# Optimization experiments

Measured on AMD Instinct MI355X. Metric: run time of the kernel, lower is better.

Reference implementation:

```python
import jax, jax.numpy as jnp
import numpy as np

N_E = 1024
E_DIM = 256
BETA = 0.25
EMA_LAMBDA = 0.99

def setup_inputs() -> dict:
    key = jax.random.key(0)
    k1, k2 = jax.random.split(key)
    z = jax.random.normal(k1, (32, 2048, E_DIM), dtype=jnp.float32)
    # torch init: uniform(-1/n_e, 1/n_e)
    embedding = jax.random.uniform(k2, (N_E, E_DIM), dtype=jnp.float32,
                                   minval=-1.0 / N_E, maxval=1.0 / N_E)
    N_t = jnp.zeros((N_E,), dtype=jnp.float32)
    m_t = jnp.zeros((N_E, E_DIM), dtype=jnp.float32)
    return {"z": z, "embedding": embedding, "N_t": N_t, "m_t": m_t}

def reference(z, embedding, N_t, m_t):
    zf = z.reshape(-1, E_DIM)  # [N, e_dim]
    # squared L2 distances: ||z||^2 + ||e||^2 - 2 z e^T  -> [N, n_e]
    d = (jnp.sum(zf * zf, axis=1, keepdims=True)
         + jnp.sum(embedding * embedding, axis=1)
         - 2.0 * jnp.matmul(zf, embedding.T))
    idx = jnp.argmin(d, axis=1)  # [N] int

    # EMA statistics (torch does a python loop over unique indices; this is the
    # vectorized equivalent: only codes that were selected get updated).
    counts = jax.ops.segment_sum(jnp.ones_like(idx, dtype=jnp.float32), idx, num_segments=N_E)
    sums = jax.ops.segment_sum(zf, idx, num_segments=N_E)  # [n_e, e_dim]
    selected = counts > 0
    N_t_new = jnp.where(selected, N_t * EMA_LAMBDA + counts * (1.0 - EMA_LAMBDA), N_t)
    m_t_new = jnp.where(selected[:, None], m_t * EMA_LAMBDA + sums * (1.0 - EMA_LAMBDA), m_t)

    z_q = embedding[idx].reshape(z.shape)
    loss = BETA * jnp.mean((jax.lax.stop_gradient(z_q) - z) ** 2)
    z_q_st = z + jax.lax.stop_gradient(z_q - z)  # straight-through

    # perplexity from code usage histogram (== mean of one-hot encodings)
    e_mean = counts / idx.shape[0]
    perplexity = jnp.exp(-jnp.sum(e_mean * jnp.log(e_mean + 1e-10)))
    return (loss, z_q_st, idx, perplexity, N_t_new, m_t_new)
```

## Files before the change

### kernel.cpp

```cpp
#include <hip/hip_runtime.h>
#include <math.h>

#define N_ROWS  65536
#define EDIM    256
#define NE      1024
#define BETA    0.25f
#define LAMBDA  0.99f

#define MARGIN  8e-3f
#define QCAP    2048


#define O_ZQ   1
#define O_IDX  16777217
#define O_PERP 16842753
#define O_NT   16842754
#define O_MT   16843778

typedef __attribute__((ext_vector_type(8))) short short8;
typedef __attribute__((ext_vector_type(4))) float f32x4;

__device__ __forceinline__ unsigned short f2bf(float f) {
    unsigned u = __float_as_uint(f);
    return (unsigned short)((u + 0x7fffu + ((u >> 16) & 1u)) >> 16);
}

__global__ __launch_bounds__(64) void prep_b_kernel(const float* __restrict__ emb,
                                                    unsigned* __restrict__ bfrag_u32,
                                                    float* __restrict__ loss_acc,
                                                    int* __restrict__ cnt) {
    int j = blockIdx.x;
    int l = threadIdx.x;
    float4 v = ((const float4*)(emb + (size_t)j * EDIM))[l];
    unsigned lo = (unsigned)f2bf(v.x) | ((unsigned)f2bf(v.y) << 16);
    unsigned hi = (unsigned)f2bf(v.z) | ((unsigned)f2bf(v.w) << 16);
    int base = ((((j >> 4) * 8 + (l >> 3)) * 64) + ((l >> 1) & 3) * 16 + (j & 15)) * 4
             + 2 * (l & 1);
    bfrag_u32[base]     = lo;
    bfrag_u32[base + 1] = hi;
    if (l == 0) cnt[j] = 0;
    if (j == 0 && l == 0) *loss_acc = 0.0f;
}

__global__ __launch_bounds__(256) void sq_kernel(const float* __restrict__ src,
                                                 float* __restrict__ dst) {
    const int tid = threadIdx.x;
    const int grp = tid >> 4;
    const int q   = tid & 15;
    const int row = blockIdx.x * 16 + grp;
    const int h = q >> 3, j = q & 7;
    const float* __restrict__ p = src + (size_t)row * EDIM + h * 128 + j;
    float acc = __fmul_rn(p[0], p[0]);
    #pragma unroll
    for (int t = 1; t < 16; ++t) {
        float v = p[8 * t];
        acc = __fadd_rn(acc, __fmul_rn(v, v));
    }
    acc = __fadd_rn(acc, __shfl_xor(acc, 1));
    acc = __fadd_rn(acc, __shfl_xor(acc, 2));
    acc = __fadd_rn(acc, __shfl_xor(acc, 4));
    acc = __fadd_rn(acc, __shfl_xor(acc, 8));
    if (q == 0) dst[row] = acc;
}

__global__ __launch_bounds__(256, 3) void argmin_kernel(const float* __restrict__ z,
                                                        const float* __restrict__ emb,
                                                        const float4* __restrict__ bsrc,
                                                        const float* __restrict__ e_sq,
                                                        int* __restrict__ idx_out,
                                                        float* __restrict__ out_zq,
                                                        float* __restrict__ out_idx,
                                                        float* __restrict__ loss_acc,
                                                        int* __restrict__ cnt) {
    __shared__ __align__(16) float4 Bs[2048];
    __shared__ uint2 queue[QCAP];
    __shared__ unsigned long long best_s[128];
    __shared__ int   idx_s[128];
    __shared__ float zsq_s[128];
    __shared__ float rmF_s[128];
    __shared__ float lred[4];
    __shared__ int qcnt;

    const int tid  = threadIdx.x;
    const int wid  = tid >> 6, lane = tid & 63;
    const int l15  = lane & 15, lg = lane >> 4;
    const int row0 = blockIdx.x * 128;
    const int rbase = row0 + wid * 32;

    if (tid < 128) best_s[tid] = ~0ull;
    if (tid == 0) qcnt = 0;

    float4 st[8];
    #pragma unroll
    for (int i = 0; i < 8; ++i) st[i] = bsrc[tid + 256 * i];

    short8 a[2][8];
    #pragma unroll
    for (int rt = 0; rt < 2; ++rt) {
        float zs = 0.f;
        #pragma unroll
        for (int ks = 0; ks < 8; ++ks) {
            const float* zp = z + (size_t)(rbase + rt * 16 + l15) * EDIM + ks * 32 + lg * 8;
            float4 f0 = *(const float4*)zp;
            float4 f1 = *(const float4*)(zp + 4);
            zs += f0.x * f0.x + f0.y * f0.y + f0.z * f0.z + f0.w * f0.w
                + f1.x * f1.x + f1.y * f1.y + f1.z * f1.z + f1.w * f1.w;
            union { short8 s; unsigned short u[8]; } pk;
            pk.u[0] = f2bf(f0.x); pk.u[1] = f2bf(f0.y); pk.u[2] = f2bf(f0.z); pk.u[3] = f2bf(f0.w);
            pk.u[4] = f2bf(f1.x); pk.u[5] = f2bf(f1.y); pk.u[6] = f2bf(f1.z); pk.u[7] = f2bf(f1.w);
            a[rt][ks] = pk.s;
        }
        zs += __shfl_xor(zs, 16);
        zs += __shfl_xor(zs, 32);
        if (lg == 0) zsq_s[wid * 32 + rt * 16 + l15] = zs;
    }

    float rm[2][4];
    #pragma unroll
    for (int rt = 0; rt < 2; ++rt)
        #pragma unroll
        for (int r = 0; r < 4; ++r) rm[rt][r] = 1e30f;

    __syncthreads();

    for (int ch = 0; ch < 16; ++ch) {
        const int cb = ch * 64;
        #pragma unroll
        for (int i = 0; i < 8; ++i) Bs[tid + 256 * i] = st[i];
        __syncthreads();
        if (ch < 15) {
            #pragma unroll
            for (int i = 0; i < 8; ++i) st[i] = bsrc[(ch + 1) * 2048 + tid + 256 * i];
        }

        float eqs[4];
        #pragma unroll
        for (int ct = 0; ct < 4; ++ct) eqs[ct] = e_sq[cb + ct * 16 + l15];

        f32x4 acc[2][4];
        #pragma unroll
        for (int rt = 0; rt < 2; ++rt)
            #pragma unroll
            for (int ct = 0; ct < 4; ++ct) acc[rt][ct] = (f32x4){0.f, 0.f, 0.f, 0.f};

        const short8* Bv = (const short8*)Bs;
        #pragma unroll
        for (int ks = 0; ks < 8; ++ks) {
            #pragma unroll
            for (int ct = 0; ct < 4; ++ct) {
                short8 b = Bv[(ct * 8 + ks) * 64 + lane];
                acc[0][ct] = __builtin_amdgcn_mfma_f32_16x16x32_bf16(a[0][ks], b, acc[0][ct], 0, 0, 0);
                acc[1][ct] = __builtin_amdgcn_mfma_f32_16x16x32_bf16(a[1][ks], b, acc[1][ct], 0, 0, 0);
            }
        }

        #pragma unroll
        for (int rt = 0; rt < 2; ++rt) {
            #pragma unroll
            for (int r = 0; r < 4; ++r) {
                float m = __fsub_rn(eqs[0], __fmul_rn(2.0f, acc[rt][0][r]));
                #pragma unroll
                for (int ct = 1; ct < 4; ++ct) {
                    float t = __fsub_rn(eqs[ct], __fmul_rn(2.0f, acc[rt][ct][r]));
                    m = fminf(m, t);
                }
                m = fminf(m, __shfl_xor(m, 1));
                m = fminf(m, __shfl_xor(m, 2));
                m = fminf(m, __shfl_xor(m, 4));
                m = fminf(m, __shfl_xor(m, 8));
                rm[rt][r] = fminf(rm[rt][r], m);
            }
        }

        #pragma unroll
        for (int rt = 0; rt < 2; ++rt) {
            #pragma unroll
            for (int ct = 0; ct < 4; ++ct) {
                #pragma unroll
                for (int r = 0; r < 4; ++r) {
                    float t = __fsub_rn(eqs[ct], __fmul_rn(2.0f, acc[rt][ct][r]));
                    if (t <= rm[rt][r] + MARGIN) {
                        int rl  = wid * 32 + rt * 16 + lg * 4 + r;
                        int col = cb + ct * 16 + l15;
                        int s = atomicAdd(&qcnt, 1);
                        if (s < QCAP) queue[s] = make_uint2((rl << 10) | col,
                                                            __float_as_uint(t));
                    }
                }
            }
        }
        __syncthreads();
    }

    #pragma unroll
    for (int rt = 0; rt < 2; ++rt)
        #pragma unroll
        for (int r = 0; r < 4; ++r)
            if (l15 == 0) rmF_s[wid * 32 + rt * 16 + lg * 4 + r] = rm[rt][r];
    __syncthreads();

    {
        int nq = qcnt; if (nq > QCAP) nq = QCAP;
        const int g = tid >> 3, q = tid & 7;
        for (int e = g; e < nq; e += 32) {
            uint2 ent = queue[e];
            int rl = ent.x >> 10, col = ent.x & 1023;
            if (__uint_as_float(ent.y) > rmF_s[rl] + MARGIN) continue;
            const float4* zr = (const float4*)(z + (size_t)(row0 + rl) * EDIM);
            const float4* er = (const float4*)(emb + (size_t)col * EDIM);
            float ae = 0.f;
            #pragma unroll
            for (int i = 0; i < 8; ++i) {
                float4 x = zr[q + 8 * i], y = er[q + 8 * i];
                ae = __fmaf_rn(x.x, y.x, ae);
                ae = __fmaf_rn(x.y, y.y, ae);
                ae = __fmaf_rn(x.z, y.z, ae);
                ae = __fmaf_rn(x.w, y.w, ae);
            }
            ae = __fadd_rn(ae, __shfl_xor(ae, 1));
            ae = __fadd_rn(ae, __shfl_xor(ae, 2));
            ae = __fadd_rn(ae, __shfl_xor(ae, 4));
            if (q == 0) {
                float d = __fsub_rn(__fadd_rn(zsq_s[rl], e_sq[col]), __fmul_rn(2.0f, ae));
                unsigned u = __float_as_uint(d);
                u = (u & 0x80000000u) ? ~u : (u | 0x80000000u);
                unsigned long long key = ((unsigned long long)u << 32) | (unsigned)col;
                atomicMin(&best_s[rl], key);
            }
        }
    }

    __syncthreads();
    if (tid < 128) {
        unsigned long long k = best_s[tid];
        int id = (int)(k & 0xffffffffull);
        idx_out[row0 + tid] = id;
        out_idx[row0 + tid] = (float)id;
        idx_s[tid] = id;
        atomicAdd(&cnt[id], 1);
    }
    __syncthreads();

    const float4* e4 = (const float4*)emb;
    for (int i = 0; i < 32; ++i) {
        int flat = tid + i * 256;
        int r = flat >> 6, c4 = flat & 63;
        int id = idx_s[r];
        float4 e = e4[(size_t)id * 64 + c4];
        float* o = out_zq + (size_t)(row0 + r) * EDIM + c4 * 4;
        o[0] = e.x; o[1] = e.y; o[2] = e.z; o[3] = e.w;
    }

    float lp = 0.f;
    if (tid < 128) {
        unsigned m = (unsigned)(best_s[tid] >> 32);
        unsigned bits = (m & 0x80000000u) ? (m & 0x7fffffffu) : ~m;
        lp = __uint_as_float(bits);
    }
    #pragma unroll
    for (int m = 32; m; m >>= 1) lp += __shfl_down(lp, m);
    if (lane == 0) lred[wid] = lp;
    __syncthreads();
    if (tid == 0) {
        float s = lred[0] + lred[1] + lred[2] + lred[3];
        atomicAdd(loss_acc, s);
    }
}

__global__ __launch_bounds__(1024) void scan_kernel(const int* __restrict__ cnt,
                                                    const float* __restrict__ N_t,
                                                    float* __restrict__ outN,
                                                    float* __restrict__ counts_f,
                                                    int* __restrict__ offs,
                                                    int* __restrict__ cursor) {
    __shared__ int s[1024];
    const int tid = threadIdx.x;
    int c = cnt[tid];
    s[tid] = c;
    __syncthreads();
    for (int d = 1; d < 1024; d <<= 1) {
        int v = (tid >= d) ? s[tid - d] : 0;
        __syncthreads();
        s[tid] += v;
        __syncthreads();
    }
    int excl = s[tid] - c;
    offs[tid] = excl;
    cursor[tid] = excl;
    counts_f[tid] = (float)c;
    float Nold = N_t[tid];
    outN[tid] = (c > 0) ? Nold * LAMBDA + (float)c * (1.0f - LAMBDA) : Nold;
}

__global__ __launch_bounds__(256) void scatter_kernel(const int* __restrict__ idx,
                                                      int* __restrict__ cursor,
                                                      int* __restrict__ sorted) {
    int i = blockIdx.x * 256 + threadIdx.x;
    int p = atomicAdd(&cursor[idx[i]], 1);
    sorted[p] = i;
}

__global__ __launch_bounds__(256) void msum_kernel(const float* __restrict__ z,
                                                   const int* __restrict__ sorted,
                                                   const int* __restrict__ offs,
                                                   const int* __restrict__ cnt,
                                                   const float* __restrict__ m_t,
                                                   float* __restrict__ outM) {
    const int j = blockIdx.x;
    const int tid = threadIdx.x, w = tid >> 6, lane = tid & 63;
    const int n = cnt[j], start = offs[j];
    float4 acc = make_float4(0.f, 0.f, 0.f, 0.f);
    for (int e = w; e < n; e += 4) {
        float4 v = ((const float4*)(z + (size_t)sorted[start + e] * EDIM))[lane];
        acc.x += v.x; acc.y += v.y; acc.z += v.z; acc.w += v.w;
    }
    __shared__ float red[4 * 256];
    *(float4*)(red + w * 256 + lane * 4) = acc;
    __syncthreads();
    if (tid < 256) {
        float s = red[tid] + red[256 + tid] + red[512 + tid] + red[768 + tid];
        float mold = m_t[(size_t)j * EDIM + tid];
        outM[(size_t)j * EDIM + tid] = (n > 0) ? mold * LAMBDA + s * (1.0f - LAMBDA) : mold;
    }
}

__global__ __launch_bounds__(256) void final_kernel(const float* __restrict__ counts,
                                                    const float* __restrict__ loss_acc,
                                                    float* __restrict__ out_loss,
                                                    float* __restrict__ out_perp) {
    const int tid = threadIdx.x, w = tid >> 6, lane = tid & 63;
    float h = 0.f;
    for (int c = tid; c < NE; c += 256) {
        float em = counts[c] * (1.0f / (float)N_ROWS);
        h += em * logf(em + 1e-10f);
    }
    #pragma unroll
    for (int m = 32; m; m >>= 1) h += __shfl_down(h, m);
    __shared__ float red[4];
    if (lane == 0) red[w] = h;
    __syncthreads();
    if (tid == 0) {
        float H = red[0] + red[1] + red[2] + red[3];
        out_perp[0] = expf(-H);
        out_loss[0] = BETA * loss_acc[0] * (1.0f / (float)(N_ROWS * EDIM));
    }
}

extern "C" void kernel_launch(void* const* d_in, const int* in_sizes, int n_in,
                              void* d_out, int out_size, void* d_ws, size_t ws_size,
                              hipStream_t stream) {
    const float* z   = (const float*)d_in[0];
    const float* emb = (const float*)d_in[1];
    const float* N_t = (const float*)d_in[2];
    const float* m_t = (const float*)d_in[3];
    float* out = (float*)d_out;
    float* ws  = (float*)d_ws;

    float* loss_acc   = ws;
    float* e_sq       = ws + 64;
    unsigned* bfrag_u = (unsigned*)(ws + 67584);
    int*   sorted     = (int*)(ws + 198656);
    int*   idx1       = (int*)(ws + 264192);
    float* counts     = ws + 329728;
    int*   cnt_i      = (int*)(ws + 330752);
    int*   offs_i     = (int*)(ws + 331776);
    int*   cursor_i   = (int*)(ws + 332800);

    prep_b_kernel<<<NE, 64, 0, stream>>>(emb, bfrag_u, loss_acc, cnt_i);
    sq_kernel<<<NE / 16, 256, 0, stream>>>(emb, e_sq);
    argmin_kernel<<<N_ROWS / 128, 256, 0, stream>>>(z, emb, (const float4*)bfrag_u,
                                                    e_sq, idx1,
                                                    out + O_ZQ, out + O_IDX, loss_acc, cnt_i);
    scan_kernel<<<1, 1024, 0, stream>>>(cnt_i, N_t, out + O_NT, counts, offs_i, cursor_i);
    scatter_kernel<<<N_ROWS / 256, 256, 0, stream>>>(idx1, cursor_i, sorted);
    msum_kernel<<<NE, 256, 0, stream>>>(z, sorted, offs_i, cnt_i, m_t, out + O_MT);
    final_kernel<<<1, 256, 0, stream>>>(counts, loss_acc, out, out + O_PERP);
}
```

Baseline: 342.6 us.

## Halve argmin row tile to 64 rows and widen msum to 512 threads

The argmin kernel now gives each wave 16 rows instead of 32, so each block covers 64 rows and twice as many blocks are launched. This cuts per-thread accumulator and A-fragment registers but halves reuse of each shared-memory codebook chunk across rows. The z_q gather is rewritten as a per-row coalesced copy, and the loss reduction is simplified to a single wave. msum now uses 8 waves per code instead of 4 to parallelise the segment sums more.

After: 367.6 us. 1.07x slower.

```diff
diff --git a/kernel.cpp b/kernel.cpp
--- a/kernel.cpp
+++ b/kernel.cpp
@@ -74,33 +74,31 @@
                                                         int* __restrict__ cnt) {
     __shared__ __align__(16) float4 Bs[2048];
     __shared__ uint2 queue[QCAP];
-    __shared__ unsigned long long best_s[128];
-    __shared__ int   idx_s[128];
-    __shared__ float zsq_s[128];
-    __shared__ float rmF_s[128];
-    __shared__ float lred[4];
+    __shared__ unsigned long long best_s[64];
+    __shared__ int   idx_s[64];
+    __shared__ float zsq_s[64];
+    __shared__ float rmF_s[64];
     __shared__ int qcnt;
 
     const int tid  = threadIdx.x;
     const int wid  = tid >> 6, lane = tid & 63;
     const int l15  = lane & 15, lg = lane >> 4;
-    const int row0 = blockIdx.x * 128;
-    const int rbase = row0 + wid * 32;
-
-    if (tid < 128) best_s[tid] = ~0ull;
+    const int row0 = blockIdx.x * 64;
+    const int rbase = row0 + wid * 16;
+
+    if (tid < 64) best_s[tid] = ~0ull;
     if (tid == 0) qcnt = 0;
 
     float4 st[8];
     #pragma unroll
     for (int i = 0; i < 8; ++i) st[i] = bsrc[tid + 256 * i];
 
-    short8 a[2][8];
-    #pragma unroll
-    for (int rt = 0; rt < 2; ++rt) {
+    short8 a[8];
+    {
         float zs = 0.f;
         #pragma unroll
         for (int ks = 0; ks < 8; ++ks) {
-            const float* zp = z + (size_t)(rbase + rt * 16 + l15) * EDIM + ks * 32 + lg * 8;
+            const float* zp = z + (size_t)(rbase + l15) * EDIM + ks * 32 + lg * 8;
             float4 f0 = *(const float4*)zp;
             float4 f1 = *(const float4*)(zp + 4);
             zs += f0.x * f0.x + f0.y * f0.y + f0.z * f0.z + f0.w * f0.w
@@ -108,18 +106,16 @@
             union { short8 s; unsigned short u[8]; } pk;
             pk.u[0] = f2bf(f0.x); pk.u[1] = f2bf(f0.y); pk.u[2] = f2bf(f0.z); pk.u[3] = f2bf(f0.w);
             pk.u[4] = f2bf(f1.x); pk.u[5] = f2bf(f1.y); pk.u[6] = f2bf(f1.z); pk.u[7] = f2bf(f1.w);
-            a[rt][ks] = pk.s;
+            a[ks] = pk.s;
         }
         zs += __shfl_xor(zs, 16);
         zs += __shfl_xor(zs, 32);
-        if (lg == 0) zsq_s[wid * 32 + rt * 16 + l15] = zs;
-    }
-
-    float rm[2][4];
-    #pragma unroll
-    for (int rt = 0; rt < 2; ++rt)
-        #pragma unroll
-        for (int r = 0; r < 4; ++r) rm[rt][r] = 1e30f;
+        if (lg == 0) zsq_s[wid * 16 + l15] = zs;
+    }
+
+    float rm[4];
+    #pragma unroll
+    for (int r = 0; r < 4; ++r) rm[r] = 1e30f;
 
     __syncthreads();
 
@@ -137,11 +133,9 @@
         #pragma unroll
         for (int ct = 0; ct < 4; ++ct) eqs[ct] = e_sq[cb + ct * 16 + l15];
 
-        f32x4 acc[2][4];
-        #pragma unroll
-        for (int rt = 0; rt < 2; ++rt)
-            #pragma unroll
-            for (int ct = 0; ct < 4; ++ct) acc[rt][ct] = (f32x4){0.f, 0.f, 0.f, 0.f};
+        f32x4 acc[4];
+        #pragma unroll
+        for (int ct = 0; ct < 4; ++ct) acc[ct] = (f32x4){0.f, 0.f, 0.f, 0.f};
 
         const short8* Bv = (const short8*)Bs;
         #pragma unroll
@@ -149,54 +143,45 @@
             #pragma unroll
             for (int ct = 0; ct < 4; ++ct) {
                 short8 b = Bv[(ct * 8 + ks) * 64 + lane];
-                acc[0][ct] = __builtin_amdgcn_mfma_f32_16x16x32_bf16(a[0][ks], b, acc[0][ct], 0, 0, 0);
-                acc[1][ct] = __builtin_amdgcn_mfma_f32_16x16x32_bf16(a[1][ks], b, acc[1][ct], 0, 0, 0);
-            }
-        }
-
-        #pragma unroll
-        for (int rt = 0; rt < 2; ++rt) {
+                acc[ct] = __builtin_amdgcn_mfma_f32_16x16x32_bf16(a[ks], b, acc[ct], 0, 0, 0);
+            }
+        }
+
+        #pragma unroll
+        for (int r = 0; r < 4; ++r) {
+            float m = __fsub_rn(eqs[0], __fmul_rn(2.0f, acc[0][r]));
+            #pragma unroll
+            for (int ct = 1; ct < 4; ++ct) {
+                float t = __fsub_rn(eqs[ct], __fmul_rn(2.0f, acc[ct][r]));
+                m = fminf(m, t);
+            }
+            m = fminf(m, __shfl_xor(m, 1));
+            m = fminf(m, __shfl_xor(m, 2));
+            m = fminf(m, __shfl_xor(m, 4));
+            m = fminf(m, __shfl_xor(m, 8));
+            rm[r] = fminf(rm[r], m);
+        }
+
+        #pragma unroll
+        for (int ct = 0; ct < 4; ++ct) {
             #pragma unroll
             for (int r = 0; r < 4; ++r) {
-                float m = __fsub_rn(eqs[0], __fmul_rn(2.0f, acc[rt][0][r]));
-                #pragma unroll
-                for (int ct = 1; ct < 4; ++ct) {
-                    float t = __fsub_rn(eqs[ct], __fmul_rn(2.0f, acc[rt][ct][r]));
-                    m = fminf(m, t);
+                float t = __fsub_rn(eqs[ct], __fmul_rn(2.0f, acc[ct][r]));
+                if (t <= rm[r] + MARGIN) {
+                    int rl  = wid * 16 + lg * 4 + r;
+                    int col = cb + ct * 16 + l15;
+                    int s = atomicAdd(&qcnt, 1);
+                    if (s < QCAP) queue[s] = make_uint2((rl << 10) | col,
+                                                        __float_as_uint(t));
                 }
-                m = fminf(m, __shfl_xor(m, 1));
-                m = fminf(m, __shfl_xor(m, 2));
-                m = fminf(m, __shfl_xor(m, 4));
-                m = fminf(m, __shfl_xor(m, 8));
-                rm[rt][r] = fminf(rm[rt][r], m);
-            }
-        }
-
-        #pragma unroll
-        for (int rt = 0; rt < 2; ++rt) {
-            #pragma unroll
-            for (int ct = 0; ct < 4; ++ct) {
-                #pragma unroll
-                for (int r = 0; r < 4; ++r) {
-                    float t = __fsub_rn(eqs[ct], __fmul_rn(2.0f, acc[rt][ct][r]));
-                    if (t <= rm[rt][r] + MARGIN) {
-                        int rl  = wid * 32 + rt * 16 + lg * 4 + r;
-                        int col = cb + ct * 16 + l15;
-                        int s = atomicAdd(&qcnt, 1);
-                        if (s < QCAP) queue[s] = make_uint2((rl << 10) | col,
-                                                            __float_as_uint(t));
-                    }
-                }
             }
         }
         __syncthreads();
     }
 
     #pragma unroll
-    for (int rt = 0; rt < 2; ++rt)
-        #pragma unroll
-        for (int r = 0; r < 4; ++r)
-            if (l15 == 0) rmF_s[wid * 32 + rt * 16 + lg * 4 + r] = rm[rt][r];
+    for (int r = 0; r < 4; ++r)
+        if (l15 == 0) rmF_s[wid * 16 + lg * 4 + r] = rm[r];
     __syncthreads();
 
     {
@@ -231,7 +216,7 @@
     }
 
     __syncthreads();
-    if (tid < 128) {
+    if (tid < 64) {
         unsigned long long k = best_s[tid];
         int id = (int)(k & 0xffffffffull);
         idx_out[row0 + tid] = id;
@@ -241,29 +226,18 @@
     }
     __syncthreads();
 
-    const float4* e4 = (const float4*)emb;
-    for (int i = 0; i < 32; ++i) {
-        int flat = tid + i * 256;
-        int r = flat >> 6, c4 = flat & 63;
-        int id = idx_s[r];
-        float4 e = e4[(size_t)id * 64 + c4];
-        float* o = out_zq + (size_t)(row0 + r) * EDIM + c4 * 4;
-        o[0] = e.x; o[1] = e.y; o[2] = e.z; o[3] = e.w;
-    }
-
-    float lp = 0.f;
-    if (tid < 128) {
-        unsigned m = (unsigned)(best_s[tid] >> 32);
+    for (int i = 0; i < 64; ++i) {
+        int id = idx_s[i];
+        out_zq[(size_t)(row0 + i) * EDIM + tid] = emb[(size_t)id * EDIM + tid];
+    }
+
+    if (wid == 0) {
+        unsigned m = (unsigned)(best_s[lane] >> 32);
         unsigned bits = (m & 0x80000000u) ? (m & 0x7fffffffu) : ~m;
-        lp = __uint_as_float(bits);
-    }
-    #pragma unroll
-    for (int m = 32; m; m >>= 1) lp += __shfl_down(lp, m);
-    if (lane == 0) lred[wid] = lp;
-    __syncthreads();
-    if (tid == 0) {
-        float s = lred[0] + lred[1] + lred[2] + lred[3];
-        atomicAdd(loss_acc, s);
+        float lp = __uint_as_float(bits);
+        #pragma unroll
+        for (int mm = 32; mm; mm >>= 1) lp += __shfl_down(lp, mm);
+        if (lane == 0) atomicAdd(loss_acc, lp);
     }
 }
 
@@ -300,7 +274,7 @@
     sorted[p] = i;
 }
 
-__global__ __launch_bounds__(256) void msum_kernel(const float* __restrict__ z,
+__global__ __launch_bounds__(512) void msum_kernel(const float* __restrict__ z,
                                                    const int* __restrict__ sorted,
                                                    const int* __restrict__ offs,
                                                    const int* __restrict__ cnt,
@@ -310,15 +284,17 @@
     const int tid = threadIdx.x, w = tid >> 6, lane = tid & 63;
     const int n = cnt[j], start = offs[j];
     float4 acc = make_float4(0.f, 0.f, 0.f, 0.f);
-    for (int e = w; e < n; e += 4) {
+    for (int e = w; e < n; e += 8) {
         float4 v = ((const float4*)(z + (size_t)sorted[start + e] * EDIM))[lane];
         acc.x += v.x; acc.y += v.y; acc.z += v.z; acc.w += v.w;
     }
-    __shared__ float red[4 * 256];
+    __shared__ float red[8 * 256];
     *(float4*)(red + w * 256 + lane * 4) = acc;
     __syncthreads();
     if (tid < 256) {
-        float s = red[tid] + red[256 + tid] + red[512 + tid] + red[768 + tid];
+        float s = 0.f;
+        #pragma unroll
+        for (int ww = 0; ww < 8; ++ww) s += red[ww * 256 + tid];
         float mold = m_t[(size_t)j * EDIM + tid];
         outM[(size_t)j * EDIM + tid] = (n > 0) ? mold * LAMBDA + s * (1.0f - LAMBDA) : mold;
     }
@@ -368,11 +344,11 @@
 
     prep_b_kernel<<<NE, 64, 0, stream>>>(emb, bfrag_u, loss_acc, cnt_i);
     sq_kernel<<<NE / 16, 256, 0, stream>>>(emb, e_sq);
-    argmin_kernel<<<N_ROWS / 128, 256, 0, stream>>>(z, emb, (const float4*)bfrag_u,
-                                                    e_sq, idx1,
-                                                    out + O_ZQ, out + O_IDX, loss_acc, cnt_i);
+    argmin_kernel<<<N_ROWS / 64, 256, 0, stream>>>(z, emb, (const float4*)bfrag_u,
+                                                   e_sq, idx1,
+                                                   out + O_ZQ, out + O_IDX, loss_acc, cnt_i);
     scan_kernel<<<1, 1024, 0, stream>>>(cnt_i, N_t, out + O_NT, counts, offs_i, cursor_i);
     scatter_kernel<<<N_ROWS / 256, 256, 0, stream>>>(idx1, cursor_i, sorted);
-    msum_kernel<<<NE, 256, 0, stream>>>(z, sorted, offs_i, cnt_i, m_t, out + O_MT);
+    msum_kernel<<<NE, 512, 0, stream>>>(z, sorted, offs_i, cnt_i, m_t, out + O_MT);
     final_kernel<<<1, 256, 0, stream>>>(counts, loss_acc, out, out + O_PERP);
 }
```
